# Kernel tuning notes

Hardware: AMD Instinct MI355X
Metric: run time of the kernel (lower is better)

Reference implementation:

```python
import jax, jax.numpy as jnp
import numpy as np

K_SELECT = 100      # select_box_nums_for_evaluation
IOU_THR = 0.7       # nms_iou_threshold
CONF_THR = 0.3      # confidence_score


def setup_inputs() -> dict:
    key = jax.random.key(0)
    k1, k2, k3 = jax.random.split(key, 3)
    B, Q, C = 256, 900, 91
    pred_logits = jax.random.normal(k1, (B, Q, C), dtype=jnp.float32)
    # cxcywh boxes in (0,1), strictly positive w/h
    pred_boxes = jax.random.uniform(k2, (B, Q, 4), dtype=jnp.float32, minval=0.05, maxval=0.45)
    # (img_h, img_w) per image
    target_sizes = jax.random.uniform(k3, (B, 2), dtype=jnp.float32, minval=200.0, maxval=1000.0)
    return {"pred_logits": pred_logits, "pred_boxes": pred_boxes, "target_sizes": target_sizes}


def _pairwise_iou(boxes):
    # boxes: [K,4] xyxy -> iou [K,K]
    area = (boxes[:, 2] - boxes[:, 0]) * (boxes[:, 3] - boxes[:, 1])
    lt = jnp.maximum(boxes[:, None, :2], boxes[None, :, :2])
    rb = jnp.minimum(boxes[:, None, 2:], boxes[None, :, 2:])
    wh = jnp.clip(rb - lt, 0.0)
    inter = wh[..., 0] * wh[..., 1]
    union = area[:, None] + area[None, :] - inter
    return inter / jnp.maximum(union, 1e-9)


def _nms_mask(boxes):
    # boxes already sorted by descending score (top_k output order).
    # Greedy NMS: box i suppresses lower-scored j if iou > IOU_THR and i itself kept.
    K = boxes.shape[0]
    iou = _pairwise_iou(boxes)
    rng = jnp.arange(K)

    def body(i, keep):
        suppress = (iou[i] > IOU_THR) & keep[i] & (rng > i)
        return keep & ~suppress

    return jax.lax.fori_loop(0, K, body, jnp.ones((K,), dtype=bool))


def reference(pred_logits, pred_boxes, target_sizes):
    B, Q, C = pred_logits.shape
    prob = jax.nn.sigmoid(pred_logits).reshape(B, Q * C)
    scores, topk_idx = jax.lax.top_k(prob, K_SELECT)        # [B,K] sorted desc
    topk_boxes = topk_idx // C                               # query index
    labels = topk_idx % C                                    # class index

    # cxcywh -> xyxy
    cxcy, wh = pred_boxes[..., :2], pred_boxes[..., 2:]
    xyxy = jnp.concatenate([cxcy - 0.5 * wh, cxcy + 0.5 * wh], axis=-1)  # [B,Q,4]
    boxes = jnp.take_along_axis(xyxy, topk_boxes[..., None], axis=1)     # [B,K,4]

    img_h, img_w = target_sizes[:, 0], target_sizes[:, 1]
    scale_fct = jnp.stack([img_w, img_h, img_w, img_h], axis=1)          # [B,4]
    boxes = boxes * scale_fct[:, None, :]

    conf_keep = scores > CONF_THR                            # confidence filter
    nms_keep = jax.vmap(_nms_mask)(boxes)                    # per-image NMS
    keep = conf_keep & nms_keep                              # fixed-shape mask (ragged lists in torch)
    return scores, labels, boxes, keep
```

## Files before the change

kernel.cpp:

```cpp
#include <hip/hip_runtime.h>
#include <stdint.h>

#define NBATCH 256
#define NQ 900
#define NC 91
#define NQC (NQ * NC)
#define KSEL 100
#define IOU_THRF 0.7f
#define CONF_THRF 0.3f
#define TH_LOGIT 2.2f
#define DELTA 4096u

#define SLC 15
#define SF4 1365
#define ANT 256
#define SCAP 128
#define CAPB (SLC * SCAP)

#define BNT 512
#define HBINS 64
#define SRTCAP 512

__device__ __forceinline__ uint32_t fkey(float x) {
  uint32_t b = __float_as_uint(x);
  return b ^ ((uint32_t)((int32_t)b >> 31) | 0x80000000u);
}
__device__ __forceinline__ float unfkey(uint32_t k) {
  uint32_t b = (k & 0x80000000u) ? (k ^ 0x80000000u) : ~k;
  return __uint_as_float(b);
}
__device__ __forceinline__ float sigmoidf_ref(float x) {
  return 1.0f / (1.0f + expf(-x));
}

__global__ __launch_bounds__(ANT) void kfilter(const float* __restrict__ logits,
                                               uint32_t* __restrict__ cnts,
                                               uint32_t* __restrict__ cand) {
  __shared__ uint32_t lbuf[SCAP];
  __shared__ uint32_t lcnt;

  const int blk = blockIdx.x;
  const int b = blk / SLC;
  const int s = blk - b * SLC;
  const int tid = threadIdx.x;
  const float4* lg4 = (const float4*)(logits + (size_t)b * NQC) + (size_t)s * SF4;

  if (tid == 0) lcnt = 0;
  __syncthreads();

  for (int i = tid; i < SF4; i += ANT) {
    float4 v = lg4[i];
    const uint32_t ibase = (uint32_t)((s * SF4 + i) * 4);
    if (v.x >= TH_LOGIT) { uint32_t p = atomicAdd(&lcnt, 1u); if (p < SCAP) lbuf[p] = ibase + 0; }
    if (v.y >= TH_LOGIT) { uint32_t p = atomicAdd(&lcnt, 1u); if (p < SCAP) lbuf[p] = ibase + 1; }
    if (v.z >= TH_LOGIT) { uint32_t p = atomicAdd(&lcnt, 1u); if (p < SCAP) lbuf[p] = ibase + 2; }
    if (v.w >= TH_LOGIT) { uint32_t p = atomicAdd(&lcnt, 1u); if (p < SCAP) lbuf[p] = ibase + 3; }
  }
  __syncthreads();
  const uint32_t m = lcnt;
  if (tid == 0) cnts[blk] = m;
  const uint32_t mw = m < SCAP ? m : SCAP;
  for (uint32_t i = tid; i < mw; i += ANT)
    cand[(size_t)blk * SCAP + i] = lbuf[i];
}

union BSMem {
  struct {
    uint32_t idxs[CAPB];
    uint32_t keys[CAPB];
    unsigned long long srt[SRTCAP];
  } p;
  struct {
    float iou[KSEL * KSEL];
    float box[KSEL][4];
    int keep[KSEL];
  } nms;
};

__global__ __launch_bounds__(BNT) void merge_nms(const uint32_t* __restrict__ cnts,
                                                 const uint32_t* __restrict__ cand,
                                                 const float* __restrict__ logits,
                                                 const float* __restrict__ pboxes,
                                                 const float* __restrict__ tsizes,
                                                 float* __restrict__ out,
                                                 int force_fallback) {
  __shared__ BSMem sm;
  __shared__ uint32_t scnt[SLC], soff[SLC];
  __shared__ uint32_t s_hist[HBINS];
  __shared__ uint32_t s_n, s_bad, s_cut, s_m;
  __shared__ unsigned long long red[BNT / 64];
  __shared__ unsigned long long s_last;

  const int b = blockIdx.x;
  const int tid = threadIdx.x;
  const float* lg = logits + (size_t)b * NQC;
  unsigned long long* ranked = (unsigned long long*)sm.p.idxs;

  bool good = !force_fallback;
  if (good) {
    if (tid < SLC) scnt[tid] = cnts[b * SLC + tid];
    __syncthreads();
    if (tid == 0) {
      uint32_t off = 0, bad = 0;
      for (int i = 0; i < SLC; i++) {
        soff[i] = off;
        if (scnt[i] > SCAP) bad = 1;
        off += scnt[i];
      }
      s_n = off;
      s_bad = bad | (off < KSEL ? 1u : 0u);
    }
    __syncthreads();
    good = (s_bad == 0);
  }
  const uint32_t n = good ? s_n : 0;

  if (good) {
    const int wid = tid >> 6, lane = tid & 63;
    for (int sl = wid; sl < SLC; sl += BNT / 64) {
      const uint32_t c = scnt[sl], o = soff[sl];
      for (uint32_t j = lane; j < c; j += 64)
        sm.p.idxs[o + j] = cand[((size_t)b * SLC + sl) * SCAP + j];
    }
    if (tid < HBINS) s_hist[tid] = 0;
    if (tid == 0) s_m = 0;
    __syncthreads();

    for (uint32_t i = tid; i < n; i += BNT) {
      uint32_t k = fkey(lg[sm.p.idxs[i]]);
      sm.p.keys[i] = k;
      uint32_t bin = (k >> 20) - 0xC00u;
      if (bin > HBINS - 1) bin = HBINS - 1;
      atomicAdd(&s_hist[bin], 1u);
    }
    __syncthreads();

    if (tid < 64) {
      uint32_t h = s_hist[tid];
      uint32_t suf = h;
      #pragma unroll
      for (int off = 1; off < 64; off <<= 1) {
        uint32_t t = __shfl_down(suf, off);
        if (tid + off < 64) suf += t;
      }
      bool pred = (suf >= KSEL) && (suf - h < KSEL);
      unsigned long long mask = __ballot(pred);
      int cutlane = __ffsll((long long)mask) - 1;
      if (tid == 0) s_cut = (uint32_t)cutlane;
    }
    __syncthreads();
    const uint32_t cut = s_cut;
    if (cut >= HBINS - 1) good = false;
    const uint32_t thresh = ((cut + 0xC00u) << 20) - DELTA;

    if (good) {
      for (uint32_t i = tid; i < n; i += BNT) {
        uint32_t k = sm.p.keys[i];
        if (k >= thresh) {
          uint32_t pb = __float_as_uint(sigmoidf_ref(unfkey(k)));
          uint32_t pos = atomicAdd(&s_m, 1u);
          if (pos < SRTCAP)
            sm.p.srt[pos] = (((unsigned long long)(~pb)) << 32) |
                            (unsigned long long)sm.p.idxs[i];
        }
      }
      __syncthreads();
      const uint32_t m = s_m;
      if (m > SRTCAP) good = false;
      if (good) {
        for (uint32_t q = tid; q < m; q += BNT) {
          unsigned long long mykey = sm.p.srt[q];
          uint32_t r = 0;
          for (uint32_t j = 0; j < m; j++)
            r += (sm.p.srt[j] < mykey) ? 1u : 0u;
          if (r < KSEL) ranked[r] = mykey;
        }
        __syncthreads();
      }
    }
  }

  if (!good) {
    unsigned long long last = ~0ULL;
    for (int r = 0; r < KSEL; r++) {
      unsigned long long best = 0ULL;
      for (int i = tid; i < NQC; i += BNT) {
        uint32_t pb = __float_as_uint(sigmoidf_ref(lg[i]));
        unsigned long long cmp = (((unsigned long long)pb) << 32) |
                                 (unsigned long long)(~(uint32_t)i);
        if (cmp < last && cmp > best) best = cmp;
      }
      #pragma unroll
      for (int o = 32; o >= 1; o >>= 1) {
        unsigned long long other = __shfl_down(best, o);
        if (other > best) best = other;
      }
      if ((tid & 63) == 0) red[tid >> 6] = best;
      __syncthreads();
      if (tid == 0) {
        unsigned long long mx = red[0];
        for (int w = 1; w < BNT / 64; w++) if (red[w] > mx) mx = red[w];
        s_last = mx;
        uint32_t pb = (uint32_t)(mx >> 32);
        uint32_t id = ~(uint32_t)mx;
        ranked[r] = (((unsigned long long)(~pb)) << 32) | (unsigned long long)id;
      }
      __syncthreads();
      last = s_last;
    }
  }

  float score = 0.0f;
  int idx = 0;
  if (tid < KSEL) {
    unsigned long long key = ranked[tid];
    score = __uint_as_float(~(uint32_t)(key >> 32));
    idx = (int)(uint32_t)(key & 0xFFFFFFFFu);
  }
  __syncthreads();

  const float img_h = tsizes[b * 2 + 0];
  const float img_w = tsizes[b * 2 + 1];
  float* out_scores = out;
  float* out_labels = out + (size_t)NBATCH * KSEL;
  float* out_boxes  = out + (size_t)2 * NBATCH * KSEL;
  float* out_keep   = out + (size_t)2 * NBATCH * KSEL + (size_t)NBATCH * KSEL * 4;

  if (tid < KSEL) {
    int q = idx / NC;
    int lab = idx - q * NC;
    const float* pb = pboxes + ((size_t)b * NQ + q) * 4;
    float cx = pb[0], cy = pb[1], w = pb[2], h = pb[3];
    float hw = __fmul_rn(0.5f, w), hh = __fmul_rn(0.5f, h);
    float x0 = __fmul_rn(__fsub_rn(cx, hw), img_w);
    float y0 = __fmul_rn(__fsub_rn(cy, hh), img_h);
    float x1 = __fmul_rn(__fadd_rn(cx, hw), img_w);
    float y1 = __fmul_rn(__fadd_rn(cy, hh), img_h);
    out_scores[(size_t)b * KSEL + tid] = score;
    out_labels[(size_t)b * KSEL + tid] = (float)lab;
    float* ob = out_boxes + ((size_t)b * KSEL + tid) * 4;
    ob[0] = x0; ob[1] = y0; ob[2] = x1; ob[3] = y1;
    sm.nms.box[tid][0] = x0; sm.nms.box[tid][1] = y0;
    sm.nms.box[tid][2] = x1; sm.nms.box[tid][3] = y1;
  }
  __syncthreads();

  for (int e = tid; e < KSEL * KSEL; e += BNT) {
    int i = e / KSEL;
    int j = e - i * KSEL;
    float ax0 = sm.nms.box[i][0], ay0 = sm.nms.box[i][1];
    float ax1 = sm.nms.box[i][2], ay1 = sm.nms.box[i][3];
    float bx0 = sm.nms.box[j][0], by0 = sm.nms.box[j][1];
    float bx1 = sm.nms.box[j][2], by1 = sm.nms.box[j][3];
    float areaA = __fmul_rn(__fsub_rn(ax1, ax0), __fsub_rn(ay1, ay0));
    float areaB = __fmul_rn(__fsub_rn(bx1, bx0), __fsub_rn(by1, by0));
    float ltx = fmaxf(ax0, bx0), lty = fmaxf(ay0, by0);
    float rbx = fminf(ax1, bx1), rby = fminf(ay1, by1);
    float wx = fmaxf(__fsub_rn(rbx, ltx), 0.0f);
    float wy = fmaxf(__fsub_rn(rby, lty), 0.0f);
    float inter = __fmul_rn(wx, wy);
    float uni = __fsub_rn(__fadd_rn(areaA, areaB), inter);
    sm.nms.iou[e] = __fdiv_rn(inter, fmaxf(uni, 1e-9f));
  }
  __syncthreads();

  if (tid < 64) {
    int keepA = 1;
    int keepB = 1;
    for (int i = 0; i < KSEL; i++) {
      int owner = i & 63;
      int ki = (i < 64) ? __shfl(keepA, owner) : __shfl(keepB, owner);
      if (ki) {
        if (tid > i && sm.nms.iou[i * KSEL + tid] > IOU_THRF) keepA = 0;
        int j = tid + 64;
        if (j < KSEL && j > i && sm.nms.iou[i * KSEL + j] > IOU_THRF) keepB = 0;
      }
    }
    sm.nms.keep[tid] = keepA;
    if (tid + 64 < KSEL) sm.nms.keep[tid + 64] = keepB;
  }
  __syncthreads();

  if (tid < KSEL) {
    float kp = (score > CONF_THRF && sm.nms.keep[tid]) ? 1.0f : 0.0f;
    out_keep[(size_t)b * KSEL + tid] = kp;
  }
}

extern "C" void kernel_launch(void* const* d_in, const int* in_sizes, int n_in,
                              void* d_out, int out_size, void* d_ws, size_t ws_size,
                              hipStream_t stream) {
  const float* logits = (const float*)d_in[0];
  const float* pboxes = (const float*)d_in[1];
  const float* tsizes = (const float*)d_in[2];
  (void)in_sizes; (void)n_in; (void)out_size;

  const size_t cnt_bytes = ((size_t)NBATCH * SLC * sizeof(uint32_t) + 255) & ~(size_t)255;
  const size_t need = cnt_bytes + (size_t)NBATCH * SLC * SCAP * sizeof(uint32_t);
  if (ws_size >= need) {
    uint32_t* cnts = (uint32_t*)d_ws;
    uint32_t* cand = (uint32_t*)((char*)d_ws + cnt_bytes);
    kfilter<<<NBATCH * SLC, ANT, 0, stream>>>(logits, cnts, cand);
    merge_nms<<<NBATCH, BNT, 0, stream>>>(cnts, cand, logits, pboxes, tsizes,
                                          (float*)d_out, 0);
  } else {
    merge_nms<<<NBATCH, BNT, 0, stream>>>(nullptr, nullptr, logits, pboxes, tsizes,
                                          (float*)d_out, 1);
  }
}
```

Measured before the change: 52.58 us.

## Carry logit keys with candidate indices and use fewer, larger filter slices

```diff
diff --git a/kernel.cpp b/kernel.cpp
--- a/kernel.cpp
+++ b/kernel.cpp
@@ -11,10 +11,11 @@
 #define TH_LOGIT 2.2f
 #define DELTA 4096u
 
-#define SLC 15
-#define SF4 1365
+#define SLC 8
+#define SF4FULL 2560
+#define SF4LAST 2555
 #define ANT 256
-#define SCAP 128
+#define SCAP 256
 #define CAPB (SLC * SCAP)
 
 #define BNT 512
@@ -35,26 +36,39 @@
 
 __global__ __launch_bounds__(ANT) void kfilter(const float* __restrict__ logits,
                                                uint32_t* __restrict__ cnts,
-                                               uint32_t* __restrict__ cand) {
-  __shared__ uint32_t lbuf[SCAP];
+                                               unsigned long long* __restrict__ cand) {
+  __shared__ unsigned long long lbuf[SCAP];
   __shared__ uint32_t lcnt;
 
   const int blk = blockIdx.x;
   const int b = blk / SLC;
   const int s = blk - b * SLC;
   const int tid = threadIdx.x;
-  const float4* lg4 = (const float4*)(logits + (size_t)b * NQC) + (size_t)s * SF4;
+  const int sf4 = (s == SLC - 1) ? SF4LAST : SF4FULL;
+  const float4* lg4 = (const float4*)(logits + (size_t)b * NQC) + (size_t)s * SF4FULL;
 
   if (tid == 0) lcnt = 0;
   __syncthreads();
 
-  for (int i = tid; i < SF4; i += ANT) {
+  for (int i = tid; i < sf4; i += ANT) {
     float4 v = lg4[i];
-    const uint32_t ibase = (uint32_t)((s * SF4 + i) * 4);
-    if (v.x >= TH_LOGIT) { uint32_t p = atomicAdd(&lcnt, 1u); if (p < SCAP) lbuf[p] = ibase + 0; }
-    if (v.y >= TH_LOGIT) { uint32_t p = atomicAdd(&lcnt, 1u); if (p < SCAP) lbuf[p] = ibase + 1; }
-    if (v.z >= TH_LOGIT) { uint32_t p = atomicAdd(&lcnt, 1u); if (p < SCAP) lbuf[p] = ibase + 2; }
-    if (v.w >= TH_LOGIT) { uint32_t p = atomicAdd(&lcnt, 1u); if (p < SCAP) lbuf[p] = ibase + 3; }
+    const uint32_t ibase = (uint32_t)((s * SF4FULL + i) * 4);
+    if (v.x >= TH_LOGIT) {
+      uint32_t p = atomicAdd(&lcnt, 1u);
+      if (p < SCAP) lbuf[p] = (((unsigned long long)fkey(v.x)) << 32) | (ibase + 0);
+    }
+    if (v.y >= TH_LOGIT) {
+      uint32_t p = atomicAdd(&lcnt, 1u);
+      if (p < SCAP) lbuf[p] = (((unsigned long long)fkey(v.y)) << 32) | (ibase + 1);
+    }
+    if (v.z >= TH_LOGIT) {
+      uint32_t p = atomicAdd(&lcnt, 1u);
+      if (p < SCAP) lbuf[p] = (((unsigned long long)fkey(v.z)) << 32) | (ibase + 2);
+    }
+    if (v.w >= TH_LOGIT) {
+      uint32_t p = atomicAdd(&lcnt, 1u);
+      if (p < SCAP) lbuf[p] = (((unsigned long long)fkey(v.w)) << 32) | (ibase + 3);
+    }
   }
   __syncthreads();
   const uint32_t m = lcnt;
@@ -66,9 +80,9 @@
 
 union BSMem {
   struct {
-    uint32_t idxs[CAPB];
-    uint32_t keys[CAPB];
+    unsigned long long keys[CAPB];
     unsigned long long srt[SRTCAP];
+    unsigned long long ranked[KSEL];
   } p;
   struct {
     float iou[KSEL * KSEL];
@@ -78,13 +92,14 @@
 };
 
 __global__ __launch_bounds__(BNT) void merge_nms(const uint32_t* __restrict__ cnts,
-                                                 const uint32_t* __restrict__ cand,
+                                                 const unsigned long long* __restrict__ cand,
                                                  const float* __restrict__ logits,
                                                  const float* __restrict__ pboxes,
                                                  const float* __restrict__ tsizes,
                                                  float* __restrict__ out,
                                                  int force_fallback) {
   __shared__ BSMem sm;
+  __shared__ unsigned long long rankbuf[KSEL];
   __shared__ uint32_t scnt[SLC], soff[SLC];
   __shared__ uint32_t s_hist[HBINS];
   __shared__ uint32_t s_n, s_bad, s_cut, s_m;
@@ -94,7 +109,6 @@
   const int b = blockIdx.x;
   const int tid = threadIdx.x;
   const float* lg = logits + (size_t)b * NQC;
-  unsigned long long* ranked = (unsigned long long*)sm.p.idxs;
 
   bool good = !force_fallback;
   if (good) {
@@ -120,15 +134,14 @@
     for (int sl = wid; sl < SLC; sl += BNT / 64) {
       const uint32_t c = scnt[sl], o = soff[sl];
       for (uint32_t j = lane; j < c; j += 64)
-        sm.p.idxs[o + j] = cand[((size_t)b * SLC + sl) * SCAP + j];
+        sm.p.keys[o + j] = cand[((size_t)b * SLC + sl) * SCAP + j];
     }
     if (tid < HBINS) s_hist[tid] = 0;
     if (tid == 0) s_m = 0;
     __syncthreads();
 
     for (uint32_t i = tid; i < n; i += BNT) {
-      uint32_t k = fkey(lg[sm.p.idxs[i]]);
-      sm.p.keys[i] = k;
+      uint32_t k = (uint32_t)(sm.p.keys[i] >> 32);
       uint32_t bin = (k >> 20) - 0xC00u;
       if (bin > HBINS - 1) bin = HBINS - 1;
       atomicAdd(&s_hist[bin], 1u);
@@ -155,13 +168,14 @@
 
     if (good) {
       for (uint32_t i = tid; i < n; i += BNT) {
-        uint32_t k = sm.p.keys[i];
+        unsigned long long key = sm.p.keys[i];
+        uint32_t k = (uint32_t)(key >> 32);
         if (k >= thresh) {
           uint32_t pb = __float_as_uint(sigmoidf_ref(unfkey(k)));
           uint32_t pos = atomicAdd(&s_m, 1u);
           if (pos < SRTCAP)
             sm.p.srt[pos] = (((unsigned long long)(~pb)) << 32) |
-                            (unsigned long long)sm.p.idxs[i];
+                            (key & 0xFFFFFFFFULL);
         }
       }
       __syncthreads();
@@ -173,7 +187,7 @@
           uint32_t r = 0;
           for (uint32_t j = 0; j < m; j++)
             r += (sm.p.srt[j] < mykey) ? 1u : 0u;
-          if (r < KSEL) ranked[r] = mykey;
+          if (r < KSEL) rankbuf[r] = mykey;
         }
         __syncthreads();
       }
@@ -203,7 +217,7 @@
         s_last = mx;
         uint32_t pb = (uint32_t)(mx >> 32);
         uint32_t id = ~(uint32_t)mx;
-        ranked[r] = (((unsigned long long)(~pb)) << 32) | (unsigned long long)id;
+        rankbuf[r] = (((unsigned long long)(~pb)) << 32) | (unsigned long long)id;
       }
       __syncthreads();
       last = s_last;
@@ -213,7 +227,7 @@
   float score = 0.0f;
   int idx = 0;
   if (tid < KSEL) {
-    unsigned long long key = ranked[tid];
+    unsigned long long key = rankbuf[tid];
     score = __uint_as_float(~(uint32_t)(key >> 32));
     idx = (int)(uint32_t)(key & 0xFFFFFFFFu);
   }
@@ -296,10 +310,11 @@
   (void)in_sizes; (void)n_in; (void)out_size;
 
   const size_t cnt_bytes = ((size_t)NBATCH * SLC * sizeof(uint32_t) + 255) & ~(size_t)255;
-  const size_t need = cnt_bytes + (size_t)NBATCH * SLC * SCAP * sizeof(uint32_t);
+  const size_t need = cnt_bytes +
+                      (size_t)NBATCH * SLC * SCAP * sizeof(unsigned long long);
   if (ws_size >= need) {
     uint32_t* cnts = (uint32_t*)d_ws;
-    uint32_t* cand = (uint32_t*)((char*)d_ws + cnt_bytes);
+    unsigned long long* cand = (unsigned long long*)((char*)d_ws + cnt_bytes);
     kfilter<<<NBATCH * SLC, ANT, 0, stream>>>(logits, cnts, cand);
     merge_nms<<<NBATCH, BNT, 0, stream>>>(cnts, cand, logits, pboxes, tsizes,
                                           (float*)d_out, 0);
```

Result: faster. 47.54 us (-9.6%).
